# Performance work log

Hardware: AMD Instinct MI355X
Metric: run time of the kernel (lower is better)

## Reference

```python
import jax, jax.numpy as jnp
import numpy as np

IN = 4096   # input_size * 2 (is_bichar)
H = 2048    # hidden_size
C = 4096    # number of lexicon inputs


def setup_inputs() -> dict:
    key = jax.random.key(0)
    ks = jax.random.split(key, 12)
    s = 0.02
    return {
        "x": jax.random.normal(ks[0], (1, IN), jnp.float32),
        "c_input": jax.random.normal(ks[1], (C, H), jnp.float32),
        "h0": jax.random.normal(ks[2], (1, H), jnp.float32),
        "c0": jax.random.normal(ks[3], (1, H), jnp.float32),
        "W_ih": jax.random.normal(ks[4], (4 * H, IN), jnp.float32) * s,
        "b_ih": jnp.zeros((4 * H,), jnp.float32),
        "W_hh": jax.random.normal(ks[5], (4 * H, H), jnp.float32) * s,
        "b_hh": jnp.zeros((4 * H,), jnp.float32),
        "aW_ih": jax.random.normal(ks[6], (H, IN), jnp.float32) * s,
        "ab_ih": jnp.zeros((H,), jnp.float32),
        "aW_hh": jax.random.normal(ks[7], (H, H), jnp.float32) * s,
        "ab_hh": jnp.zeros((H,), jnp.float32),
    }


def reference(x, c_input, h0, c0, W_ih, b_ih, W_hh, b_hh, aW_ih, ab_ih, aW_hh, ab_hh):
    # gate pre-activations: [1, 4H]
    lstm_vec = x @ W_ih.T + b_ih + h0 @ W_hh.T + b_hh
    i, f, o, g = jnp.split(lstm_vec, 4, axis=1)
    i = jax.nn.sigmoid(i)
    f = jax.nn.sigmoid(f + 1.0)  # computed but unused when lexicon is non-empty (faithful)
    g = jnp.tanh(g)
    o = jax.nn.sigmoid(o)
    # alpha over lexicon entries: [C, H] (x-projection broadcasts over C)
    alpha = jax.nn.sigmoid(x @ aW_ih.T + ab_ih + c_input @ aW_hh.T + ab_hh)
    # exp-normalize over the (C+1) candidates per hidden unit
    w = jnp.exp(jnp.concatenate([i, alpha], axis=0))  # [C+1, H]
    w = w / w.sum(axis=0)
    merge = jnp.concatenate([g, c_input], axis=0)  # [C+1, H]
    c1 = (merge * w).sum(axis=0, keepdims=True)  # [1, H]
    h1 = o * jnp.tanh(c1)
    return h1, c1
```

## Files before the change

### kernel.cpp

```cpp
#include <hip/hip_runtime.h>
#include <hip/hip_bf16.h>
#include <cstdint>

#define HDIM 2048
#define INDIM 4096
#define CDIM 4096
#define KDIM 2048

typedef __attribute__((ext_vector_type(4))) int int4v;

__device__ __forceinline__ void gload16(const void* g, void* l) {
  __builtin_amdgcn_global_load_lds(
      (const __attribute__((address_space(1))) void*)g,
      (__attribute__((address_space(3))) void*)l, 16, 0, 0);
}

__global__ __launch_bounds__(256) void k_quant_xa2(
    const float* __restrict__ c_input, const float* __restrict__ aW_hh,
    int8_t* __restrict__ a8, int8_t* __restrict__ b8,
    float* __restrict__ dAs, float* __restrict__ dBs,
    const float* __restrict__ x,
    const float* __restrict__ aW_ih, const float* __restrict__ ab_ih,
    const float* __restrict__ ab_hh,
    float* __restrict__ xa2, float* __restrict__ accz) {
  const int t = threadIdx.x;
  const int wid = t >> 6, lane = t & 63;

  if (blockIdx.x < 1536) {
    if (blockIdx.x == 0) {
#pragma unroll
      for (int i = 0; i < 16; ++i) accz[i * 256 + t] = 0.f;
    }
    const int row = blockIdx.x * 4 + wid;
    const float* src; int8_t* dst; float* dsc; int r;
    if (row < CDIM) { src = c_input; dst = a8; dsc = dAs; r = row; }
    else            { src = aW_hh;  dst = b8; dsc = dBs; r = row - CDIM; }
    const float4* s4 = (const float4*)(src + (size_t)r * KDIM);
    float4 v[8];
#pragma unroll
    for (int it = 0; it < 8; ++it) v[it] = s4[it * 64 + lane];
    float am = 0.f;
#pragma unroll
    for (int it = 0; it < 8; ++it)
      am = fmaxf(am, fmaxf(fmaxf(fabsf(v[it].x), fabsf(v[it].y)),
                           fmaxf(fabsf(v[it].z), fabsf(v[it].w))));
#pragma unroll
    for (int off = 32; off > 0; off >>= 1) am = fmaxf(am, __shfl_xor(am, off));
    am = fmaxf(am, 1e-20f);
    const float inv = 127.0f / am;
    uint32_t* qd = (uint32_t*)(dst + (size_t)r * KDIM);
#pragma unroll
    for (int it = 0; it < 8; ++it) {
      uint32_t p = (uint32_t)(__float2int_rn(v[it].x * inv) & 0xFF)
                 | ((uint32_t)(__float2int_rn(v[it].y * inv) & 0xFF) << 8)
                 | ((uint32_t)(__float2int_rn(v[it].z * inv) & 0xFF) << 16)
                 | ((uint32_t)(__float2int_rn(v[it].w * inv) & 0xFF) << 24);
      qd[it * 64 + lane] = p;
    }
    if (lane == 0) dsc[r] = am * (1.0f / 127.0f);
    return;
  }

  const int h = (blockIdx.x - 1536) * 4 + wid;
  const float4* x4 = (const float4*)x;
  const float4* wr4 = (const float4*)(aW_ih + (size_t)h * INDIM);
  float sum = 0.f;
#pragma unroll
  for (int g = 0; g < 2; ++g) {
    float4 w[8];
#pragma unroll
    for (int it = 0; it < 8; ++it) w[it] = wr4[(g * 8 + it) * 64 + lane];
#pragma unroll
    for (int it = 0; it < 8; ++it) {
      float4 xv = x4[(g * 8 + it) * 64 + lane];
      sum += w[it].x * xv.x + w[it].y * xv.y + w[it].z * xv.z + w[it].w * xv.w;
    }
  }
#pragma unroll
  for (int off = 32; off > 0; off >>= 1) sum += __shfl_down(sum, off);
  if (lane == 0) xa2[h] = sum + ab_ih[h] + ab_hh[h];
}

__global__ __launch_bounds__(256, 4) void k_gemm_gemv(
    const int8_t* __restrict__ A, const int8_t* __restrict__ B,
    const float* __restrict__ dAs, const float* __restrict__ dBs,
    const float* __restrict__ c_in, const float* __restrict__ xa2,
    float* __restrict__ acc_se, float* __restrict__ acc_sce,
    const float* __restrict__ x, const float* __restrict__ h0,
    const float* __restrict__ W_ih, const float* __restrict__ b_ih,
    const float* __restrict__ W_hh, const float* __restrict__ b_hh,
    float* __restrict__ i_sig, float* __restrict__ o_sig,
    float* __restrict__ g_tanh) {
  __shared__ uint8_t As[2][8192];
  __shared__ uint8_t Bs[2][8192];
  const int t = threadIdx.x;
  const int lane = t & 63, wid = t >> 6;

  if (blockIdx.x < 512) {
    const int wr = wid >> 1, wc = wid & 1;
    const int l15 = lane & 15, l4 = lane >> 4;
    const int bid = blockIdx.x;
    const int bn = (bid & 7) * 2 + ((bid >> 3) & 1);
    const int bm = bid >> 4;
    const int m0 = bm * 128, n0 = bn * 128;

    int4v acc[4][4] = {};

    const int trow = t >> 2;
    const int tcol = (((t & 3) ^ ((trow >> 1) & 3)) * 16);
    const int8_t* Arow = A + (size_t)(m0 + trow) * KDIM + tcol;
    const int8_t* Brow = B + (size_t)(n0 + trow) * KDIM + tcol;

#define STAGE(buf, k0)                                                          \
    do {                                                                        \
      _Pragma("unroll")                                                         \
      for (int qq = 0; qq < 2; ++qq) {                                          \
        gload16(Arow + (size_t)qq * 64 * KDIM + (k0), As[buf] + qq * 4096 + t * 16); \
        gload16(Brow + (size_t)qq * 64 * KDIM + (k0), Bs[buf] + qq * 4096 + t * 16); \
      }                                                                         \
    } while (0)

    STAGE(0, 0);
    __syncthreads();

    int cur = 0;
    for (int ti = 0; ti < KDIM / 64; ++ti) {
      if (ti < KDIM / 64 - 1) STAGE(cur ^ 1, (ti + 1) * 64);
      int4v af[4], bfr[4];
#pragma unroll
      for (int m = 0; m < 4; ++m) {
        const int r = wr * 64 + m * 16 + l15;
        af[m] = *(const int4v*)(As[cur] + r * 64 + ((l4 ^ ((r >> 1) & 3)) * 16));
      }
#pragma unroll
      for (int n = 0; n < 4; ++n) {
        const int r = wc * 64 + n * 16 + l15;
        bfr[n] = *(const int4v*)(Bs[cur] + r * 64 + ((l4 ^ ((r >> 1) & 3)) * 16));
      }
#pragma unroll
      for (int m = 0; m < 4; ++m)
#pragma unroll
        for (int n = 0; n < 4; ++n)
          acc[m][n] = __builtin_amdgcn_mfma_i32_16x16x64_i8(af[m], bfr[n], acc[m][n], 0, 0, 0);
      __syncthreads();
      cur ^= 1;
    }
#undef STAGE

#pragma unroll
    for (int n = 0; n < 4; ++n) {
      const int hcol = n0 + wc * 64 + n * 16 + l15;
      const float xa = xa2[hcol];
      const float db = dBs[hcol];
      float se = 0.f, sce = 0.f;
#pragma unroll
      for (int m = 0; m < 4; ++m) {
        const int jbase = m0 + wr * 64 + m * 16 + l4 * 4;
#pragma unroll
        for (int rr = 0; rr < 4; ++rr) {
          const float sc = dAs[jbase + rr] * db;
          float z = (float)acc[m][n][rr] * sc + xa;
          float s = 1.f / (1.f + __expf(-z));
          float e = __expf(s);
          se += e;
          sce += c_in[(size_t)(jbase + rr) * HDIM + hcol] * e;
        }
      }
      se += __shfl_xor(se, 16); se += __shfl_xor(se, 32);
      sce += __shfl_xor(sce, 16); sce += __shfl_xor(sce, 32);
      if (l4 == 0) {
        atomicAdd(&acc_se[hcol], se);
        atomicAdd(&acc_sce[hcol], sce);
      }
    }
    return;
  }

  const int vr = (blockIdx.x - 512) * 4 + wid;
  const int typ = vr >> 11;
  const int h = vr & (HDIM - 1);
  const int grow = (typ == 0) ? h : (typ == 1) ? (2 * HDIM + h) : (3 * HDIM + h);
  float sum = 0.f;
  const float4* x4 = (const float4*)x;
  const float4* wr4 = (const float4*)(W_ih + (size_t)grow * INDIM);
#pragma unroll
  for (int g = 0; g < 2; ++g) {
    float4 w[8];
#pragma unroll
    for (int it = 0; it < 8; ++it) w[it] = wr4[(g * 8 + it) * 64 + lane];
#pragma unroll
    for (int it = 0; it < 8; ++it) {
      float4 xv = x4[(g * 8 + it) * 64 + lane];
      sum += w[it].x * xv.x + w[it].y * xv.y + w[it].z * xv.z + w[it].w * xv.w;
    }
  }
  {
    const float4* wh4 = (const float4*)(W_hh + (size_t)grow * HDIM);
    const float4* h4 = (const float4*)h0;
    float4 w[8];
#pragma unroll
    for (int it = 0; it < 8; ++it) w[it] = wh4[it * 64 + lane];
#pragma unroll
    for (int it = 0; it < 8; ++it) {
      float4 hv = h4[it * 64 + lane];
      sum += w[it].x * hv.x + w[it].y * hv.y + w[it].z * hv.z + w[it].w * hv.w;
    }
  }
#pragma unroll
  for (int off = 32; off > 0; off >>= 1) sum += __shfl_down(sum, off);
  if (lane == 0) {
    float z = sum + b_ih[grow] + b_hh[grow];
    if (typ == 0)      i_sig[h] = 1.f / (1.f + expf(-z));
    else if (typ == 1) o_sig[h] = 1.f / (1.f + expf(-z));
    else               g_tanh[h] = tanhf(z);
  }
}

__global__ __launch_bounds__(256) void k_final(
    const float* __restrict__ i_sig, const float* __restrict__ o_sig,
    const float* __restrict__ g_tanh, const float* __restrict__ acc_se,
    const float* __restrict__ acc_sce, float* __restrict__ out) {
  int h = blockIdx.x * 256 + threadIdx.x;
  if (h >= HDIM) return;
  float wi = expf(i_sig[h]);
  float tot = acc_se[h] + wi;
  float c1 = (acc_sce[h] + g_tanh[h] * wi) / tot;
  float h1 = o_sig[h] * tanhf(c1);
  out[h] = h1;
  out[HDIM + h] = c1;
}

extern "C" void kernel_launch(void* const* d_in, const int* in_sizes, int n_in,
                              void* d_out, int out_size, void* d_ws, size_t ws_size,
                              hipStream_t stream) {
  const float* x     = (const float*)d_in[0];
  const float* c_inp = (const float*)d_in[1];
  const float* h0    = (const float*)d_in[2];
  const float* W_ih  = (const float*)d_in[4];
  const float* b_ih  = (const float*)d_in[5];
  const float* W_hh  = (const float*)d_in[6];
  const float* b_hh  = (const float*)d_in[7];
  const float* aW_ih = (const float*)d_in[8];
  const float* ab_ih = (const float*)d_in[9];
  const float* aW_hh = (const float*)d_in[10];
  const float* ab_hh = (const float*)d_in[11];
  float* out = (float*)d_out;

  char* ws = (char*)d_ws;
  int8_t* a8 = (int8_t*)ws;
  int8_t* b8 = a8 + (size_t)CDIM * KDIM;
  float* dAs = (float*)(b8 + (size_t)HDIM * KDIM);
  float* dBs = dAs + CDIM;
  float* fb  = dBs + HDIM;
  float* i_sig   = fb;
  float* o_sig   = fb + HDIM;
  float* g_tanh  = fb + 2 * HDIM;
  float* xa2     = fb + 3 * HDIM;
  float* acc_se  = fb + 4 * HDIM;
  float* acc_sce = fb + 5 * HDIM;

  k_quant_xa2<<<2048, 256, 0, stream>>>(
      c_inp, aW_hh, a8, b8, dAs, dBs, x, aW_ih, ab_ih, ab_hh, xa2, acc_se);
  k_gemm_gemv<<<512 + 1536, 256, 0, stream>>>(
      a8, b8, dAs, dBs, c_inp, xa2, acc_se, acc_sce,
      x, h0, W_ih, b_ih, W_hh, b_hh, i_sig, o_sig, g_tanh);
  k_final<<<(HDIM + 255) / 256, 256, 0, stream>>>(i_sig, o_sig, g_tanh,
                                                  acc_se, acc_sce, out);
}
```

Baseline: 66.52 us.

## Move W_hh gate GEMV into prep kernel and pin load waits

Moves the h0·W_hh part of the LSTM gate pre-activations, with its biases, from the gemm/gemv kernel into the first prep kernel. The partial sums go to a new workspace buffer, gate_part, and the second kernel adds them to its W_ih GEMV, which now issues 16 float4 loads per lane at once. The aim is to balance memory traffic across the two kernels and shorten the critical second kernel. It also inserts explicit s_waitcnt vmcnt(0) after batched loads so all loads are issued before use. The cost is 1536 extra blocks in the prep launch and more registers in the gemv path.

```diff
diff --git a/kernel.cpp b/kernel.cpp
--- a/kernel.cpp
+++ b/kernel.cpp
@@ -15,14 +15,19 @@
       (__attribute__((address_space(3))) void*)l, 16, 0, 0);
 }
 
-__global__ __launch_bounds__(256) void k_quant_xa2(
+#define LOADPIN() asm volatile("s_waitcnt vmcnt(0)" ::: "memory")
+
+__global__ __launch_bounds__(256) void k_prep(
     const float* __restrict__ c_input, const float* __restrict__ aW_hh,
     int8_t* __restrict__ a8, int8_t* __restrict__ b8,
     float* __restrict__ dAs, float* __restrict__ dBs,
-    const float* __restrict__ x,
+    const float* __restrict__ x, const float* __restrict__ h0,
     const float* __restrict__ aW_ih, const float* __restrict__ ab_ih,
     const float* __restrict__ ab_hh,
-    float* __restrict__ xa2, float* __restrict__ accz) {
+    const float* __restrict__ W_hh, const float* __restrict__ b_ih,
+    const float* __restrict__ b_hh,
+    float* __restrict__ xa2, float* __restrict__ gate_part,
+    float* __restrict__ accz) {
   const int t = threadIdx.x;
   const int wid = t >> 6, lane = t & 63;
 
@@ -39,6 +44,7 @@
     float4 v[8];
 #pragma unroll
     for (int it = 0; it < 8; ++it) v[it] = s4[it * 64 + lane];
+    LOADPIN();
     float am = 0.f;
 #pragma unroll
     for (int it = 0; it < 8; ++it)
@@ -61,24 +67,50 @@
     return;
   }
 
-  const int h = (blockIdx.x - 1536) * 4 + wid;
-  const float4* x4 = (const float4*)x;
-  const float4* wr4 = (const float4*)(aW_ih + (size_t)h * INDIM);
+  if (blockIdx.x < 2048) {
+    const int h = (blockIdx.x - 1536) * 4 + wid;
+    const float4* x4 = (const float4*)x;
+    const float4* wr4 = (const float4*)(aW_ih + (size_t)h * INDIM);
+    float sum = 0.f;
+#pragma unroll
+    for (int g = 0; g < 2; ++g) {
+      float4 w[8];
+#pragma unroll
+      for (int it = 0; it < 8; ++it) w[it] = wr4[(g * 8 + it) * 64 + lane];
+      LOADPIN();
+#pragma unroll
+      for (int it = 0; it < 8; ++it) {
+        float4 xv = x4[(g * 8 + it) * 64 + lane];
+        sum += w[it].x * xv.x + w[it].y * xv.y + w[it].z * xv.z + w[it].w * xv.w;
+      }
+    }
+#pragma unroll
+    for (int off = 32; off > 0; off >>= 1) sum += __shfl_down(sum, off);
+    if (lane == 0) xa2[h] = sum + ab_ih[h] + ab_hh[h];
+    return;
+  }
+
+  const int vr = (blockIdx.x - 2048) * 4 + wid;
+  const int typ = vr >> 11;
+  const int h = vr & (HDIM - 1);
+  const int grow = (typ == 0) ? h : (typ == 1) ? (2 * HDIM + h) : (3 * HDIM + h);
+  const float4* wh4 = (const float4*)(W_hh + (size_t)grow * HDIM);
+  const float4* h4 = (const float4*)h0;
   float sum = 0.f;
-#pragma unroll
-  for (int g = 0; g < 2; ++g) {
+  {
     float4 w[8];
 #pragma unroll
-    for (int it = 0; it < 8; ++it) w[it] = wr4[(g * 8 + it) * 64 + lane];
+    for (int it = 0; it < 8; ++it) w[it] = wh4[it * 64 + lane];
+    LOADPIN();
 #pragma unroll
     for (int it = 0; it < 8; ++it) {
-      float4 xv = x4[(g * 8 + it) * 64 + lane];
-      sum += w[it].x * xv.x + w[it].y * xv.y + w[it].z * xv.z + w[it].w * xv.w;
+      float4 hv = h4[it * 64 + lane];
+      sum += w[it].x * hv.x + w[it].y * hv.y + w[it].z * hv.z + w[it].w * hv.w;
     }
   }
 #pragma unroll
   for (int off = 32; off > 0; off >>= 1) sum += __shfl_down(sum, off);
-  if (lane == 0) xa2[h] = sum + ab_ih[h] + ab_hh[h];
+  if (lane == 0) gate_part[vr] = sum + b_ih[grow] + b_hh[grow];
 }
 
 __global__ __launch_bounds__(256, 4) void k_gemm_gemv(
@@ -86,9 +118,8 @@
     const float* __restrict__ dAs, const float* __restrict__ dBs,
     const float* __restrict__ c_in, const float* __restrict__ xa2,
     float* __restrict__ acc_se, float* __restrict__ acc_sce,
-    const float* __restrict__ x, const float* __restrict__ h0,
-    const float* __restrict__ W_ih, const float* __restrict__ b_ih,
-    const float* __restrict__ W_hh, const float* __restrict__ b_hh,
+    const float* __restrict__ x, const float* __restrict__ W_ih,
+    const float* __restrict__ gate_part,
     float* __restrict__ i_sig, float* __restrict__ o_sig,
     float* __restrict__ g_tanh) {
   __shared__ uint8_t As[2][8192];
@@ -180,36 +211,24 @@
   const int typ = vr >> 11;
   const int h = vr & (HDIM - 1);
   const int grow = (typ == 0) ? h : (typ == 1) ? (2 * HDIM + h) : (3 * HDIM + h);
-  float sum = 0.f;
   const float4* x4 = (const float4*)x;
   const float4* wr4 = (const float4*)(W_ih + (size_t)grow * INDIM);
-#pragma unroll
-  for (int g = 0; g < 2; ++g) {
-    float4 w[8];
-#pragma unroll
-    for (int it = 0; it < 8; ++it) w[it] = wr4[(g * 8 + it) * 64 + lane];
-#pragma unroll
-    for (int it = 0; it < 8; ++it) {
-      float4 xv = x4[(g * 8 + it) * 64 + lane];
+  float sum = 0.f;
+  {
+    float4 w[16];
+#pragma unroll
+    for (int it = 0; it < 16; ++it) w[it] = wr4[it * 64 + lane];
+    LOADPIN();
+#pragma unroll
+    for (int it = 0; it < 16; ++it) {
+      float4 xv = x4[it * 64 + lane];
       sum += w[it].x * xv.x + w[it].y * xv.y + w[it].z * xv.z + w[it].w * xv.w;
-    }
-  }
-  {
-    const float4* wh4 = (const float4*)(W_hh + (size_t)grow * HDIM);
-    const float4* h4 = (const float4*)h0;
-    float4 w[8];
-#pragma unroll
-    for (int it = 0; it < 8; ++it) w[it] = wh4[it * 64 + lane];
-#pragma unroll
-    for (int it = 0; it < 8; ++it) {
-      float4 hv = h4[it * 64 + lane];
-      sum += w[it].x * hv.x + w[it].y * hv.y + w[it].z * hv.z + w[it].w * hv.w;
     }
   }
 #pragma unroll
   for (int off = 32; off > 0; off >>= 1) sum += __shfl_down(sum, off);
   if (lane == 0) {
-    float z = sum + b_ih[grow] + b_hh[grow];
+    float z = sum + gate_part[vr];
     if (typ == 0)      i_sig[h] = 1.f / (1.f + expf(-z));
     else if (typ == 1) o_sig[h] = 1.f / (1.f + expf(-z));
     else               g_tanh[h] = tanhf(z);
@@ -252,18 +271,20 @@
   float* dAs = (float*)(b8 + (size_t)HDIM * KDIM);
   float* dBs = dAs + CDIM;
   float* fb  = dBs + HDIM;
-  float* i_sig   = fb;
-  float* o_sig   = fb + HDIM;
-  float* g_tanh  = fb + 2 * HDIM;
-  float* xa2     = fb + 3 * HDIM;
-  float* acc_se  = fb + 4 * HDIM;
-  float* acc_sce = fb + 5 * HDIM;
-
-  k_quant_xa2<<<2048, 256, 0, stream>>>(
-      c_inp, aW_hh, a8, b8, dAs, dBs, x, aW_ih, ab_ih, ab_hh, xa2, acc_se);
+  float* i_sig    = fb;
+  float* o_sig    = fb + HDIM;
+  float* g_tanh   = fb + 2 * HDIM;
+  float* xa2      = fb + 3 * HDIM;
+  float* acc_se   = fb + 4 * HDIM;
+  float* acc_sce  = fb + 5 * HDIM;
+  float* gate_part = fb + 6 * HDIM;
+
+  k_prep<<<3584, 256, 0, stream>>>(
+      c_inp, aW_hh, a8, b8, dAs, dBs, x, h0, aW_ih, ab_ih, ab_hh,
+      W_hh, b_ih, b_hh, xa2, gate_part, acc_se);
   k_gemm_gemv<<<512 + 1536, 256, 0, stream>>>(
       a8, b8, dAs, dBs, c_inp, xa2, acc_se, acc_sce,
-      x, h0, W_ih, b_ih, W_hh, b_hh, i_sig, o_sig, g_tanh);
+      x, W_ih, gate_part, i_sig, o_sig, g_tanh);
   k_final<<<(HDIM + 255) / 256, 256, 0, stream>>>(i_sig, o_sig, g_tanh,
                                                   acc_se, acc_sce, out);
 }
```

Measured after the change: 67.94 us. +2.1%, slower.

## Co-schedule int8 GEMM and gate GEMV waves in one triple-buffered workgroup

Applied to the files above, without the earlier changes.

Merges the int8 MFMA GEMM and the LSTM gate GEMV into 512-thread workgroups. Waves 0-3 run the GEMM with a three-stage LDS ring and explicit vmcnt waits. Waves 4-7 compute the i, o and g rows for one hidden unit each, issuing their loads between shared barriers so the two kinds of work overlap on the same CU. The epilogue now reads the quantized int8 c_input times its row scale instead of the fp32 c_input, which cuts epilogue traffic but adds quantization error to the weighted sum. The barrier count in both wave groups must stay matched, which makes the code fragile.

```diff
diff --git a/kernel.cpp b/kernel.cpp
--- a/kernel.cpp
+++ b/kernel.cpp
@@ -13,6 +13,19 @@
   __builtin_amdgcn_global_load_lds(
       (const __attribute__((address_space(1))) void*)g,
       (__attribute__((address_space(3))) void*)l, 16, 0, 0);
+}
+
+#define LOADPIN() asm volatile("s_waitcnt vmcnt(0)" ::: "memory")
+#define WAITCNT4() asm volatile("s_waitcnt vmcnt(4)" ::: "memory")
+#define WGBAR()                                   \
+  do {                                            \
+    __builtin_amdgcn_sched_barrier(0);            \
+    __builtin_amdgcn_s_barrier();                 \
+    __builtin_amdgcn_sched_barrier(0);            \
+  } while (0)
+
+__device__ __forceinline__ float dot4(float4 a, float4 b) {
+  return a.x * b.x + a.y * b.y + a.z * b.z + a.w * b.w;
 }
 
 __global__ __launch_bounds__(256) void k_quant_xa2(
@@ -39,6 +52,7 @@
     float4 v[8];
 #pragma unroll
     for (int it = 0; it < 8; ++it) v[it] = s4[it * 64 + lane];
+    LOADPIN();
     float am = 0.f;
 #pragma unroll
     for (int it = 0; it < 8; ++it)
@@ -70,36 +84,35 @@
     float4 w[8];
 #pragma unroll
     for (int it = 0; it < 8; ++it) w[it] = wr4[(g * 8 + it) * 64 + lane];
-#pragma unroll
-    for (int it = 0; it < 8; ++it) {
-      float4 xv = x4[(g * 8 + it) * 64 + lane];
-      sum += w[it].x * xv.x + w[it].y * xv.y + w[it].z * xv.z + w[it].w * xv.w;
-    }
+    LOADPIN();
+#pragma unroll
+    for (int it = 0; it < 8; ++it)
+      sum += dot4(w[it], x4[(g * 8 + it) * 64 + lane]);
   }
 #pragma unroll
   for (int off = 32; off > 0; off >>= 1) sum += __shfl_down(sum, off);
   if (lane == 0) xa2[h] = sum + ab_ih[h] + ab_hh[h];
 }
 
-__global__ __launch_bounds__(256, 4) void k_gemm_gemv(
+__global__ __launch_bounds__(512, 4) void k_fused(
     const int8_t* __restrict__ A, const int8_t* __restrict__ B,
     const float* __restrict__ dAs, const float* __restrict__ dBs,
-    const float* __restrict__ c_in, const float* __restrict__ xa2,
+    const float* __restrict__ xa2,
     float* __restrict__ acc_se, float* __restrict__ acc_sce,
     const float* __restrict__ x, const float* __restrict__ h0,
-    const float* __restrict__ W_ih, const float* __restrict__ b_ih,
-    const float* __restrict__ W_hh, const float* __restrict__ b_hh,
+    const float* __restrict__ W_ih, const float* __restrict__ W_hh,
+    const float* __restrict__ b_ih, const float* __restrict__ b_hh,
     float* __restrict__ i_sig, float* __restrict__ o_sig,
     float* __restrict__ g_tanh) {
-  __shared__ uint8_t As[2][8192];
-  __shared__ uint8_t Bs[2][8192];
+  __shared__ uint8_t As[3][8192];
+  __shared__ uint8_t Bs[3][8192];
   const int t = threadIdx.x;
   const int lane = t & 63, wid = t >> 6;
-
-  if (blockIdx.x < 512) {
+  const int bid = blockIdx.x;
+
+  if (wid < 4) {
     const int wr = wid >> 1, wc = wid & 1;
     const int l15 = lane & 15, l4 = lane >> 4;
-    const int bid = blockIdx.x;
     const int bn = (bid & 7) * 2 + ((bid >> 3) & 1);
     const int bm = bid >> 4;
     const int m0 = bm * 128, n0 = bn * 128;
@@ -111,21 +124,24 @@
     const int8_t* Arow = A + (size_t)(m0 + trow) * KDIM + tcol;
     const int8_t* Brow = B + (size_t)(n0 + trow) * KDIM + tcol;
 
-#define STAGE(buf, k0)                                                          \
+#define STAGE(buf, kt)                                                          \
     do {                                                                        \
       _Pragma("unroll")                                                         \
       for (int qq = 0; qq < 2; ++qq) {                                          \
-        gload16(Arow + (size_t)qq * 64 * KDIM + (k0), As[buf] + qq * 4096 + t * 16); \
-        gload16(Brow + (size_t)qq * 64 * KDIM + (k0), Bs[buf] + qq * 4096 + t * 16); \
+        gload16(Arow + (size_t)qq * 64 * KDIM + (size_t)(kt) * 64,              \
+                As[buf] + qq * 4096 + t * 16);                                  \
+        gload16(Brow + (size_t)qq * 64 * KDIM + (size_t)(kt) * 64,              \
+                Bs[buf] + qq * 4096 + t * 16);                                  \
       }                                                                         \
     } while (0)
 
     STAGE(0, 0);
-    __syncthreads();
-
-    int cur = 0;
-    for (int ti = 0; ti < KDIM / 64; ++ti) {
-      if (ti < KDIM / 64 - 1) STAGE(cur ^ 1, (ti + 1) * 64);
+    STAGE(1, 1);
+    WAITCNT4();
+    WGBAR();
+
+    for (int ti = 0; ti < 32; ++ti) {
+      const int cur = ti % 3;
       int4v af[4], bfr[4];
 #pragma unroll
       for (int m = 0; m < 4; ++m) {
@@ -137,13 +153,15 @@
         const int r = wc * 64 + n * 16 + l15;
         bfr[n] = *(const int4v*)(Bs[cur] + r * 64 + ((l4 ^ ((r >> 1) & 3)) * 16));
       }
+      if (ti < 30) STAGE((ti + 2) % 3, ti + 2);
 #pragma unroll
       for (int m = 0; m < 4; ++m)
 #pragma unroll
         for (int n = 0; n < 4; ++n)
           acc[m][n] = __builtin_amdgcn_mfma_i32_16x16x64_i8(af[m], bfr[n], acc[m][n], 0, 0, 0);
-      __syncthreads();
-      cur ^= 1;
+      if (ti < 30) { WAITCNT4(); }
+      else         { LOADPIN();  }
+      WGBAR();
     }
 #undef STAGE
 
@@ -158,12 +176,12 @@
         const int jbase = m0 + wr * 64 + m * 16 + l4 * 4;
 #pragma unroll
         for (int rr = 0; rr < 4; ++rr) {
-          const float sc = dAs[jbase + rr] * db;
-          float z = (float)acc[m][n][rr] * sc + xa;
+          const float da = dAs[jbase + rr];
+          float z = (float)acc[m][n][rr] * (da * db) + xa;
           float s = 1.f / (1.f + __expf(-z));
           float e = __expf(s);
           se += e;
-          sce += c_in[(size_t)(jbase + rr) * HDIM + hcol] * e;
+          sce += (float)A[(size_t)(jbase + rr) * KDIM + hcol] * (da * e);
         }
       }
       se += __shfl_xor(se, 16); se += __shfl_xor(se, 32);
@@ -176,43 +194,78 @@
     return;
   }
 
-  const int vr = (blockIdx.x - 512) * 4 + wid;
-  const int typ = vr >> 11;
-  const int h = vr & (HDIM - 1);
-  const int grow = (typ == 0) ? h : (typ == 1) ? (2 * HDIM + h) : (3 * HDIM + h);
-  float sum = 0.f;
+  const int h = bid * 4 + (wid - 4);
+  const float4* WIi = (const float4*)(W_ih + (size_t)h * INDIM);
+  const float4* WIo = (const float4*)(W_ih + (size_t)(2 * HDIM + h) * INDIM);
+  const float4* WIg = (const float4*)(W_ih + (size_t)(3 * HDIM + h) * INDIM);
+  const float4* WHi = (const float4*)(W_hh + (size_t)h * HDIM);
+  const float4* WHo = (const float4*)(W_hh + (size_t)(2 * HDIM + h) * HDIM);
+  const float4* WHg = (const float4*)(W_hh + (size_t)(3 * HDIM + h) * HDIM);
   const float4* x4 = (const float4*)x;
-  const float4* wr4 = (const float4*)(W_ih + (size_t)grow * INDIM);
-#pragma unroll
-  for (int g = 0; g < 2; ++g) {
-    float4 w[8];
-#pragma unroll
-    for (int it = 0; it < 8; ++it) w[it] = wr4[(g * 8 + it) * 64 + lane];
-#pragma unroll
-    for (int it = 0; it < 8; ++it) {
-      float4 xv = x4[(g * 8 + it) * 64 + lane];
-      sum += w[it].x * xv.x + w[it].y * xv.y + w[it].z * xv.z + w[it].w * xv.w;
-    }
-  }
-  {
-    const float4* wh4 = (const float4*)(W_hh + (size_t)grow * HDIM);
-    const float4* h4 = (const float4*)h0;
-    float4 w[8];
-#pragma unroll
-    for (int it = 0; it < 8; ++it) w[it] = wh4[it * 64 + lane];
-#pragma unroll
-    for (int it = 0; it < 8; ++it) {
-      float4 hv = h4[it * 64 + lane];
-      sum += w[it].x * hv.x + w[it].y * hv.y + w[it].z * hv.z + w[it].w * hv.w;
-    }
-  }
-#pragma unroll
-  for (int off = 32; off > 0; off >>= 1) sum += __shfl_down(sum, off);
+  const float4* h4 = (const float4*)h0;
+  float sI = 0.f, sO = 0.f, sG = 0.f;
+  float4 w[8];
+
+#define BPTR(bb) ((bb) < 6 ? ((((bb) >> 1) == 0) ? WIi : (((bb) >> 1) == 1) ? WIo : WIg) + ((bb) & 1) * 512 \
+                           : (((bb) == 6) ? WHi : ((bb) == 7) ? WHo : WHg))
+#define ISSUE(bb)                                                   \
+  do {                                                              \
+    const float4* _s = BPTR(bb);                                    \
+    _Pragma("unroll")                                               \
+    for (int it = 0; it < 8; ++it) w[it] = _s[it * 64 + lane];      \
+  } while (0)
+#define CONSUME(bb)                                                 \
+  do {                                                              \
+    LOADPIN();       \
+    _Pragma("unroll")                                               \
+    for (int it = 0; it < 8; ++it) {                                \
+      float4 _xv = ((bb) < 6) ? x4[((bb) & 1) * 512 + it * 64 + lane] \
+                              : h4[it * 64 + lane];                 \
+      float _d = dot4(w[it], _xv);                                  \
+      if (((bb) < 6 && ((bb) >> 1) == 0) || (bb) == 6) sI += _d;    \
+      else if (((bb) < 6 && ((bb) >> 1) == 1) || (bb) == 7) sO += _d; \
+      else sG += _d;                                                \
+    }                                                               \
+  } while (0)
+
+  ISSUE(0);
+  WGBAR();
+#pragma unroll
+  for (int m = 1; m <= 32; ++m) {
+    if (m % 3 == 0) {
+      const int b = m / 3 - 1;
+      switch (b) {
+        case 0: CONSUME(0); ISSUE(1); break;
+        case 1: CONSUME(1); ISSUE(2); break;
+        case 2: CONSUME(2); ISSUE(3); break;
+        case 3: CONSUME(3); ISSUE(4); break;
+        case 4: CONSUME(4); ISSUE(5); break;
+        case 5: CONSUME(5); ISSUE(6); break;
+        case 6: CONSUME(6); ISSUE(7); break;
+        case 7: CONSUME(7); ISSUE(8); break;
+        case 8: CONSUME(8); break;
+        default: break;
+      }
+    }
+    WGBAR();
+  }
+#undef BPTR
+#undef ISSUE
+#undef CONSUME
+
+#pragma unroll
+  for (int off = 32; off > 0; off >>= 1) {
+    sI += __shfl_down(sI, off);
+    sO += __shfl_down(sO, off);
+    sG += __shfl_down(sG, off);
+  }
   if (lane == 0) {
-    float z = sum + b_ih[grow] + b_hh[grow];
-    if (typ == 0)      i_sig[h] = 1.f / (1.f + expf(-z));
-    else if (typ == 1) o_sig[h] = 1.f / (1.f + expf(-z));
-    else               g_tanh[h] = tanhf(z);
+    float zI = sI + b_ih[h] + b_hh[h];
+    float zO = sO + b_ih[2 * HDIM + h] + b_hh[2 * HDIM + h];
+    float zG = sG + b_ih[3 * HDIM + h] + b_hh[3 * HDIM + h];
+    i_sig[h] = 1.f / (1.f + expf(-zI));
+    o_sig[h] = 1.f / (1.f + expf(-zO));
+    g_tanh[h] = tanhf(zG);
   }
 }
 
@@ -252,18 +305,18 @@
   float* dAs = (float*)(b8 + (size_t)HDIM * KDIM);
   float* dBs = dAs + CDIM;
   float* fb  = dBs + HDIM;
-  float* i_sig   = fb;
-  float* o_sig   = fb + HDIM;
-  float* g_tanh  = fb + 2 * HDIM;
-  float* xa2     = fb + 3 * HDIM;
-  float* acc_se  = fb + 4 * HDIM;
-  float* acc_sce = fb + 5 * HDIM;
+  float* xa2     = fb;
+  float* acc_se  = fb + HDIM;
+  float* acc_sce = fb + 2 * HDIM;
+  float* i_sig   = fb + 3 * HDIM;
+  float* o_sig   = fb + 4 * HDIM;
+  float* g_tanh  = fb + 5 * HDIM;
 
   k_quant_xa2<<<2048, 256, 0, stream>>>(
       c_inp, aW_hh, a8, b8, dAs, dBs, x, aW_ih, ab_ih, ab_hh, xa2, acc_se);
-  k_gemm_gemv<<<512 + 1536, 256, 0, stream>>>(
-      a8, b8, dAs, dBs, c_inp, xa2, acc_se, acc_sce,
-      x, h0, W_ih, b_ih, W_hh, b_hh, i_sig, o_sig, g_tanh);
+  k_fused<<<512, 512, 0, stream>>>(
+      a8, b8, dAs, dBs, xa2, acc_se, acc_sce,
+      x, h0, W_ih, W_hh, b_ih, b_hh, i_sig, o_sig, g_tanh);
   k_final<<<(HDIM + 255) / 256, 256, 0, stream>>>(i_sig, o_sig, g_tanh,
                                                   acc_se, acc_sce, out);
 }
```

Measured after the change: 103.0 us. 54.9% more time.
